# Performance work log

Hardware: AMD Instinct MI355X
Metric: run time of the kernel (lower is better)

Reference implementation:

```python
import jax, jax.numpy as jnp
import numpy as np

VOCAB, D, K = 100000, 300, 5

def setup_inputs() -> dict:
    key = jax.random.key(0)
    ks = jax.random.split(key, 12)
    B, BAG, L = 64, 16, 128
    token_ids = jax.random.randint(ks[0], (B * BAG, L), 0, VOCAB)
    mention_rep = jax.random.normal(ks[1], (B, BAG, D), dtype=jnp.float32)
    s = 0.05
    emb = jax.random.normal(ks[2], (VOCAB, D), dtype=jnp.float32)
    W1 = jax.random.normal(ks[3], (D, D), dtype=jnp.float32) * s
    b1 = jnp.zeros((D,), jnp.float32)
    conv_w = jax.random.normal(ks[4], (D, D, K), dtype=jnp.float32) * s  # [out, in, k]
    conv_b = jnp.zeros((D,), jnp.float32)
    W2 = jax.random.normal(ks[5], (2 * D, D), dtype=jnp.float32) * s
    b2 = jnp.zeros((D,), jnp.float32)
    W3 = jax.random.normal(ks[6], (D, D), dtype=jnp.float32) * s
    b3 = jnp.zeros((D,), jnp.float32)
    return {"token_ids": token_ids, "mention_rep": mention_rep, "emb": emb,
            "W1": W1, "b1": b1, "conv_w": conv_w, "conv_b": conv_b,
            "W2": W2, "b2": b2, "W3": W3, "b3": b3}

def reference(token_ids, mention_rep, emb, W1, b1, conv_w, conv_b, W2, b2, W3, b3):
    # fused gather+pad: [N, L, D]
    x = emb[token_ids]
    # lin1
    x = x @ W1 + b1
    # conv1d over time, VALID, stride 1: NCH layout
    xc = jnp.transpose(x, (0, 2, 1))  # [N, D, L]
    y = jax.lax.conv_general_dilated(xc, conv_w, (1,), 'VALID',
                                     dimension_numbers=('NCH', 'OIH', 'NCH'))
    y = y + conv_b[None, :, None]
    cnn_out = jnp.max(y, axis=-1)  # [N, D]
    m = mention_rep.reshape(mention_rep.shape[0] * mention_rep.shape[1], -1)  # dropout = identity (eval)
    concat = jnp.concatenate([cnn_out, m], axis=-1)
    h = jnp.tanh(concat @ W2 + b2)
    out = h @ W3 + b3  # dropout = identity (eval)
    return out
```

## Files before the change

### kernel.cpp

```cpp
#include <hip/hip_runtime.h>


#define DD   300
#define LL   128
#define TOUT 124
#define CH   16
#define XR   20
#define NSTG 8
#define BLK  320
#define KS     19
#define SLABP  6080
#define ROWP   20
#define WS_G1_OFF  0
#define WS_CV_OFF  194560
#define WS_NEEDED  1167360
#define NPH        114

typedef __attribute__((ext_vector_type(8))) _Float16 f16x8;
typedef __attribute__((ext_vector_type(4))) _Float16 f16x4;
typedef __attribute__((ext_vector_type(4))) float f32x4;
typedef __attribute__((ext_vector_type(16))) float f32x16;
typedef unsigned int   u32;
typedef unsigned short u16;
typedef __attribute__((ext_vector_type(4))) u32 u32x4;

__device__ __forceinline__ float b2f(u16 u) {
    union { float f; u32 i; } x; x.i = ((u32)u) << 16; return x.f;
}
__device__ __forceinline__ u16 f2bu(float f) {
    union { float f; u32 i; } x; x.f = f;
    u32 r = x.i + 0x7FFFu + ((x.i >> 16) & 1u);
    return (u16)(r >> 16);
}
__device__ __forceinline__ float ld(const void* p, size_t idx, int is32) {
    return is32 ? ((const float*)p)[idx] : b2f(((const u16*)p)[idx]);
}
__device__ __forceinline__ int sniff_is32(const void* W1) {
    int cnt = 0;
    const u32* w1raw = (const u32*)W1;
    for (int i = 0; i < 64; ++i) {
        u32 e = (w1raw[i] >> 7) & 0xFFu;
        cnt += (e >= 100u && e <= 126u) ? 1 : 0;
    }
    return (cnt < 32) ? 1 : 0;
}

__device__ __forceinline__ void barrier_lgkm() {
    asm volatile("s_waitcnt lgkmcnt(0)" ::: "memory");
    __builtin_amdgcn_s_barrier();
}

__device__ __forceinline__ void unit_decomp(int u, int& o, int& kq) {
    kq = (u >= 912) ? 3 : (u >= 608) ? 2 : (u >= 304) ? 1 : 0;
    o  = u - 304 * kq;
}
__device__ __forceinline__ void g1_load(const float* W1f, int kk, int o, int kq, float r[4]) {
    const int kbase = kk * 16 + kq * 4;
    #pragma unroll
    for (int j = 0; j < 4; ++j) {
        const int k = kbase + j;
        r[j] = (k < DD && o < DD) ? W1f[(size_t)k * DD + o] : 0.f;
    }
}
__device__ __forceinline__ void g1_write(_Float16* Ws, int o, int kq, const float r[4]) {
    f16x4 v;
    #pragma unroll
    for (int j = 0; j < 4; ++j) v[j] = (_Float16)r[j];
    *(f16x4*)&Ws[o * ROWP + (kq << 2)] = v;
}
__device__ __forceinline__ void cv_load(const float* CWf, int kk, int o, int kq, float r[20]) {
    const int kbase = kk * 16 + kq * 4;
    const bool ok = (o < DD) && (kbase < DD);
    const float4* src = (const float4*)(CWf + (size_t)o * 1500 + kk * 80 + kq * 20);
    #pragma unroll
    for (int i = 0; i < 5; ++i) {
        float4 t = ok ? src[i] : float4{0.f, 0.f, 0.f, 0.f};
        r[4*i] = t.x; r[4*i+1] = t.y; r[4*i+2] = t.z; r[4*i+3] = t.w;
    }
}
__device__ __forceinline__ void cv_write(_Float16* Ws, int o, int kq, const float r[20]) {
    #pragma unroll
    for (int s = 0; s < 5; ++s) {
        f16x4 v;
        #pragma unroll
        for (int j = 0; j < 4; ++j) v[j] = (_Float16)r[j * 5 + s];
        *(f16x4*)&Ws[s * SLABP + o * ROWP + (kq << 2)] = v;
    }
}

__global__ void CNNEncoder_36258113912977_xform(
    const void* W1, const void* conv_w, void* ws)
{
    if (!sniff_is32(W1)) return;
    const int kk = blockIdx.x, part = blockIdx.y, tid = threadIdx.x;

    if (part == 0) {
        const float* W1f = (const float*)W1;
        f16x8* dst = (f16x8*)((char*)ws + WS_G1_OFF) + (size_t)kk * 640;
        for (int g = tid; g < 640; g += 512) {
            const int kc = (g >= 320) ? 1 : 0;
            const int nn = g - kc * 320;
            f16x8 v;
            #pragma unroll
            for (int e = 0; e < 8; ++e) {
                const int k = kk * 16 + kc * 8 + e;
                v[e] = (_Float16)((k < DD && nn < DD) ? W1f[(size_t)k * DD + nn] : 0.f);
            }
            dst[g] = v;
        }
    } else {
        const int s = part - 1;
        const float* CWf = (const float*)conv_w;
        f16x8* dst = (f16x8*)((char*)ws + WS_CV_OFF) + (size_t)kk * 3200 + (size_t)s * 640;
        for (int g = tid; g < 640; g += 512) {
            const int kc = (g >= 320) ? 1 : 0;
            const int nn = g - kc * 320;
            f16x8 v;
            #pragma unroll
            for (int e = 0; e < 8; ++e) {
                const int k = kk * 16 + kc * 8 + e;
                v[e] = (_Float16)((k < DD && nn < DD)
                        ? CWf[(size_t)nn * 1500 + (size_t)k * 5 + s] : 0.f);
            }
            dst[g] = v;
        }
    }
}

#define STAGE_PH(P, Q) do {                                                 \
    if (stager) {                                                           \
        const int wr_ = (P) + 5;                                            \
        if (wr_ < NPH) *(u32x4*)&ring[(wr_ % 6) * 5120 + sg * 8] = Q;       \
        const int lp_ = (P) + 7;                                            \
        if (lp_ < NPH) Q = ((const u32x4*)ws)[(size_t)lp_ * 640 + sg];      \
    }                                                                       \
} while (0)

#define PH_BODY(P, SROW, KKC, Q) do {                                       \
    STAGE_PH((P), Q);                                                       \
    const int c_ = 2 * (KKC) + lh;                                          \
    const int row_ = mrow0 + l31 + (SROW);                                  \
    const f16x8 a_ = *(const f16x8*)&XB[row_ * 320 + ((c_ ^ (row_ & 7)) << 3)]; \
    const _Float16* bp_ = &ring[((P) % 6) * 5120 + lh * 2560];              \
    __builtin_amdgcn_s_setprio(1);                                          \
    { const f16x8 b_ = *(const f16x8*)&bp_[nn0 * 8];                        \
      acc0 = __builtin_amdgcn_mfma_f32_32x32x16_f16(a_, b_, acc0, 0, 0, 0); } \
    { const f16x8 b_ = *(const f16x8*)&bp_[nn1 * 8];                        \
      acc1 = __builtin_amdgcn_mfma_f32_32x32x16_f16(a_, b_, acc1, 0, 0, 0); } \
    if (nt3) { const f16x8 b_ = *(const f16x8*)&bp_[nn2 * 8];               \
      acc2 = __builtin_amdgcn_mfma_f32_32x32x16_f16(a_, b_, acc2, 0, 0, 0); } \
    __builtin_amdgcn_s_setprio(0);                                          \
    barrier_lgkm();                                                         \
} while (0)

#define PH_G1(KK, Q)    PH_BODY((KK), 0, (KK), Q)
#define PH_CV(KK, S, Q) PH_BODY(19 + (KK) * 5 + (S), (S), (KK), Q)

#define EPI_TILE(ACC, TILE) do {                                            \
    const int col_ = (TILE) * 32 + l31;                                     \
    const float bb_ = (col_ < DD) ? b1f[col_] : 0.f;                        \
    const int cc_ = col_ >> 3, c7_ = col_ & 7;                              \
    _Pragma("unroll")                                                       \
    for (int q_ = 0; q_ < 4; ++q_) {                                        \
        _Pragma("unroll")                                                   \
        for (int r_ = 0; r_ < 4; ++r_) {                                    \
            const int row_ = mrow0 + q_ * 8 + 4 * lh + r_;                  \
            XB[row_ * 320 + ((cc_ ^ (row_ & 7)) << 3) + c7_]                \
                = (_Float16)(ACC[4 * q_ + r_] + bb_);                       \
        } }                                                                 \
} while (0)

#define MAX_TILE(ACC, TILE) do {                                            \
    float m_ = -3.0e38f;                                                    \
    _Pragma("unroll")                                                       \
    for (int q_ = 0; q_ < 4; ++q_) {                                        \
        if (!(wm == 3 && q_ == 3)) {                                        \
            _Pragma("unroll")                                               \
            for (int r_ = 0; r_ < 4; ++r_) m_ = fmaxf(m_, ACC[4 * q_ + r_]); \
        } else if (lh == 0) {                                               \
            _Pragma("unroll")                                               \
            for (int r_ = 0; r_ < 4; ++r_) m_ = fmaxf(m_, ACC[12 + r_]);    \
        } }                                                                 \
    m_ = fmaxf(m_, __shfl_xor(m_, 32));                                     \
    if (lh == 0) pmax4[wm][(TILE) * 32 + l31] = m_;                         \
} while (0)

__global__ __launch_bounds__(1024, 4) void CNNEncoder_36258113912977_kernel(
    const int* __restrict__ tok, const void* mention, const void* emb,
    const void* W1, const void* b1, const void* conv_w, const void* conv_b,
    const void* W2, const void* b2, const void* W3, const void* b3,
    void* out, const void* ws)
{
    if (!sniff_is32(W1)) return;

    __shared__ __align__(16) _Float16 XB[132 * 320];
    __shared__ __align__(16) _Float16 ring[6 * 5120];
    __shared__ float pmax4[4][320];
    __shared__ float cbuf[2 * DD];
    __shared__ float hpart[2][DD];
    __shared__ float hbuf[DD];

    const int n = blockIdx.x, tid = threadIdx.x;
    const int w   = tid >> 6;
    const int l   = tid & 63;
    const int l31 = l & 31, lh = l >> 5;
    const int wm  = w >> 2;
    const int wn  = w & 3;
    const int mrow0 = wm * 32;
    const bool nt3 = (wn < 2);
    const int nn0 = wn * 32 + l31;
    const int nn1 = nn0 + 128;
    const int nn2 = nn0 + 256;
    const bool stager = (w < 10);
    const int sg = w * 64 + l;
    const int* trow = tok + (size_t)n * LL;

    u32x4 qE, qO;
    u32x4 pre0, pre1, pre2, pre3, pre4;

    if (stager) {
        const u32x4* wsv = (const u32x4*)ws;
        pre0 = wsv[sg];          pre1 = wsv[640 + sg];
        pre2 = wsv[1280 + sg];   pre3 = wsv[1920 + sg];
        pre4 = wsv[2560 + sg];
        qE   = wsv[3200 + sg];
        qO   = wsv[3840 + sg];
    }

    for (int i = tid; i < 132 * 160; i += 1024) ((u32*)XB)[i] = 0u;
    barrier_lgkm();

    {
        const int r = tid >> 3, q = tid & 7;
        const float* erow = (const float*)emb + (size_t)trow[r] * DD;
        for (int c = q; c < 38; c += 8) {
            f16x8 v;
            if (c < 37) {
                const float4 f0 = *(const float4*)(erow + 8 * c);
                const float4 f1 = *(const float4*)(erow + 8 * c + 4);
                v[0]=(_Float16)f0.x; v[1]=(_Float16)f0.y;
                v[2]=(_Float16)f0.z; v[3]=(_Float16)f0.w;
                v[4]=(_Float16)f1.x; v[5]=(_Float16)f1.y;
                v[6]=(_Float16)f1.z; v[7]=(_Float16)f1.w;
            } else {
                const float4 f0 = *(const float4*)(erow + 296);
                v[0]=(_Float16)f0.x; v[1]=(_Float16)f0.y;
                v[2]=(_Float16)f0.z; v[3]=(_Float16)f0.w;
                v[4]=(_Float16)0.f; v[5]=(_Float16)0.f;
                v[6]=(_Float16)0.f; v[7]=(_Float16)0.f;
            }
            const int p = c ^ (r & 7);
            *(f16x8*)&XB[r * 320 + (p << 3)] = v;
        }
    }

    if (stager) {
        *(u32x4*)&ring[0 * 5120 + sg * 8] = pre0;
        *(u32x4*)&ring[1 * 5120 + sg * 8] = pre1;
        *(u32x4*)&ring[2 * 5120 + sg * 8] = pre2;
        *(u32x4*)&ring[3 * 5120 + sg * 8] = pre3;
        *(u32x4*)&ring[4 * 5120 + sg * 8] = pre4;
    }
    barrier_lgkm();

    f32x16 acc0, acc1, acc2;
    #pragma unroll
    for (int j = 0; j < 16; ++j) { acc0[j] = 0.f; acc1[j] = 0.f; acc2[j] = 0.f; }

    for (int kk = 0; kk < 18; kk += 2) {
        PH_G1(kk,     qE);
        PH_G1(kk + 1, qO);
    }
    PH_G1(18, qE);

    {
        const float* b1f = (const float*)b1;
        EPI_TILE(acc0, wn);
        EPI_TILE(acc1, wn + 4);
        if (nt3) EPI_TILE(acc2, wn + 8);
    }
    barrier_lgkm();

    #pragma unroll
    for (int j = 0; j < 16; ++j) { acc0[j] = 0.f; acc1[j] = 0.f; acc2[j] = 0.f; }

    for (int kk = 0; kk < 18; kk += 2) {
        PH_CV(kk, 0, qO);  PH_CV(kk, 1, qE);
        PH_CV(kk, 2, qO);  PH_CV(kk, 3, qE);
        PH_CV(kk, 4, qO);
        PH_CV(kk + 1, 0, qE);  PH_CV(kk + 1, 1, qO);
        PH_CV(kk + 1, 2, qE);  PH_CV(kk + 1, 3, qO);
        PH_CV(kk + 1, 4, qE);
    }
    PH_CV(18, 0, qO);  PH_CV(18, 1, qE);
    PH_CV(18, 2, qO);  PH_CV(18, 3, qE);
    PH_CV(18, 4, qO);

    MAX_TILE(acc0, wn);
    MAX_TILE(acc1, wn + 4);
    if (nt3) MAX_TILE(acc2, wn + 8);
    __syncthreads();

    if (tid < DD) {
        float m = fmaxf(fmaxf(pmax4[0][tid], pmax4[1][tid]),
                        fmaxf(pmax4[2][tid], pmax4[3][tid]));
        cbuf[tid]      = m + ((const float*)conv_b)[tid];
        cbuf[DD + tid] = ((const float*)mention)[(size_t)n * DD + tid];
    }
    __syncthreads();

    if (tid < 2 * DD) {
        const int part = (tid >= DD) ? 1 : 0;
        const int j = tid - part * DD;
        const float* W2f = (const float*)W2;
        const int c0 = part * DD;
        float a0 = 0.f, a1 = 0.f, a2 = 0.f, a3 = 0.f;
        for (int c = c0; c < c0 + DD; c += 4) {
            a0 += cbuf[c]     * W2f[(size_t)c * DD + j];
            a1 += cbuf[c + 1] * W2f[(size_t)(c + 1) * DD + j];
            a2 += cbuf[c + 2] * W2f[(size_t)(c + 2) * DD + j];
            a3 += cbuf[c + 3] * W2f[(size_t)(c + 3) * DD + j];
        }
        hpart[part][j] = (a0 + a1) + (a2 + a3);
    }
    __syncthreads();
    if (tid < DD)
        hbuf[tid] = tanhf(((const float*)b2)[tid] + hpart[0][tid] + hpart[1][tid]);
    __syncthreads();

    if (tid < 2 * DD) {
        const int part = (tid >= DD) ? 1 : 0;
        const int j = tid - part * DD;
        const float* W3f = (const float*)W3;
        const int c0 = part * 150;
        float a0 = 0.f, a1 = 0.f;
        for (int c = c0; c < c0 + 150; c += 2) {
            a0 += hbuf[c]     * W3f[(size_t)c * DD + j];
            a1 += hbuf[c + 1] * W3f[(size_t)(c + 1) * DD + j];
        }
        hpart[part][j] = a0 + a1;
    }
    __syncthreads();
    if (tid < DD)
        ((float*)out)[(size_t)n * DD + tid]
            = ((const float*)b3)[tid] + hpart[0][tid] + hpart[1][tid];
}

__global__ __launch_bounds__(512, 2) void CNNEncoder_36258113912977_nows(
    const int* __restrict__ tok, const void* mention, const void* emb,
    const void* W1, const void* b1, const void* conv_w, const void* conv_b,
    const void* W2, const void* b2, const void* W3, const void* b3,
    void* out)
{
    if (!sniff_is32(W1)) return;

    __shared__ __align__(16) _Float16 XB[132 * 320];
    __shared__ __align__(16) _Float16 Ws[5 * SLABP];
    __shared__ float pmax2[2][304];
    __shared__ float cbuf[2 * DD];
    __shared__ float hbuf[DD];

    const int n = blockIdx.x, tid = threadIdx.x;
    const int w   = tid >> 6;
    const int l   = tid & 63;
    const int l15 = l & 15, lg = l >> 4;
    const int wm  = w >> 2;
    const int wn  = w & 3;
    const int ntw   = (wn < 3) ? 5 : 4;
    const int nbase = wn * 80;
    const int mrow0 = wm * 64;
    const int* trow = tok + (size_t)n * LL;
    const float* W1f = (const float*)W1;
    const float* CWf = (const float*)conv_w;

    int o0, kq0, o1, kq1, o2, kq2;
    unit_decomp(tid, o0, kq0);
    unit_decomp(512 + tid, o1, kq1);
    const bool act2 = (l < 24);
    unit_decomp(1024 + w * 24 + (l < 24 ? l : 0), o2, kq2);

    for (int i = tid; i < 132 * 160; i += 512) ((u32*)XB)[i] = 0u;
    __syncthreads();

    {
        const int r = tid >> 2, q = tid & 3;
        const float* erow = (const float*)emb + (size_t)trow[r] * DD;
        for (int c = q; c < 38; c += 4) {
            f16x8 v;
            if (c < 37) {
                const float4 f0 = *(const float4*)(erow + 8 * c);
                const float4 f1 = *(const float4*)(erow + 8 * c + 4);
                v[0]=(_Float16)f0.x; v[1]=(_Float16)f0.y;
                v[2]=(_Float16)f0.z; v[3]=(_Float16)f0.w;
                v[4]=(_Float16)f1.x; v[5]=(_Float16)f1.y;
                v[6]=(_Float16)f1.z; v[7]=(_Float16)f1.w;
            } else {
                const float4 f0 = *(const float4*)(erow + 296);
                v[0]=(_Float16)f0.x; v[1]=(_Float16)f0.y;
                v[2]=(_Float16)f0.z; v[3]=(_Float16)f0.w;
                v[4]=(_Float16)0.f; v[5]=(_Float16)0.f;
                v[6]=(_Float16)0.f; v[7]=(_Float16)0.f;
            }
            const int p = c ^ (r & 7);
            *(f16x8*)&XB[r * 320 + (p << 3)] = v;
        }
    }

    f32x4 acc[4][5];
    const f32x4 vzero = {0.f, 0.f, 0.f, 0.f};
    #pragma unroll
    for (int mt = 0; mt < 4; ++mt)
        #pragma unroll
        for (int nt = 0; nt < 5; ++nt) acc[mt][nt] = vzero;

    float g1a[4], g1b[4], g1c[4];
    float cfa[20], cfb[20], cfc[20];

    g1_load(W1f, 0, o0, kq0, g1a);
    g1_load(W1f, 0, o1, kq1, g1b);
    if (act2) g1_load(W1f, 0, o2, kq2, g1c);
    __syncthreads();

    for (int kk = 0; kk < KS; ++kk) {
        g1_write(Ws, o0, kq0, g1a);
        g1_write(Ws, o1, kq1, g1b);
        if (act2) g1_write(Ws, o2, kq2, g1c);
        barrier_lgkm();
        if (kk + 1 < KS) {
            g1_load(W1f, kk + 1, o0, kq0, g1a);
            g1_load(W1f, kk + 1, o1, kq1, g1b);
            if (act2) g1_load(W1f, kk + 1, o2, kq2, g1c);
        } else {
            cv_load(CWf, 0, o0, kq0, cfa);
            cv_load(CWf, 0, o1, kq1, cfb);
            if (act2) cv_load(CWf, 0, o2, kq2, cfc);
        }
        {
            f16x4 af[4];
            #pragma unroll
            for (int mt = 0; mt < 4; ++mt) {
                const int row = mrow0 + mt * 16 + l15;
                const int c = (kk << 1) + (lg >> 1);
                af[mt] = *(const f16x4*)&XB[row * 320 + ((c ^ (row & 7)) << 3) + ((lg & 1) << 2)];
            }
            #pragma unroll
            for (int nt = 0; nt < 5; ++nt) {
                if (nt < ntw) {
                    const int nn = nbase + nt * 16 + l15;
                    const f16x4 b = *(const f16x4*)&Ws[nn * ROWP + (lg << 2)];
                    #pragma unroll
                    for (int mt = 0; mt < 4; ++mt)
                        acc[mt][nt] = __builtin_amdgcn_mfma_f32_16x16x16f16(af[mt], b, acc[mt][nt], 0, 0, 0);
                }
            }
        }
        __builtin_amdgcn_s_barrier();
    }

    {
        const float* b1f = (const float*)b1;
        #pragma unroll
        for (int nt = 0; nt < 5; ++nt) {
            if (nt < ntw) {
                const int col = nbase + nt * 16 + l15;
                const float bb = (col < DD) ? b1f[col] : 0.f;
                #pragma unroll
                for (int mt = 0; mt < 4; ++mt) {
                    #pragma unroll
                    for (int j = 0; j < 4; ++j) {
                        const int row = mrow0 + mt * 16 + (lg << 2) + j;
                        XB[row * 320 + (((col >> 3) ^ (row & 7)) << 3) + (col & 7)]
                            = (_Float16)(acc[mt][nt][j] + bb);
                    }
                }
            }
        }
    }

    #pragma unroll
    for (int mt = 0; mt < 4; ++mt)
        #pragma unroll
        for (int nt = 0; nt < 5; ++nt) acc[mt][nt] = vzero;

    for (int kk = 0; kk < KS; ++kk) {
        cv_write(Ws, o0, kq0, cfa);
        cv_write(Ws, o1, kq1, cfb);
        if (act2) cv_write(Ws, o2, kq2, cfc);
        barrier_lgkm();
        if (kk + 1 < KS) {
            cv_load(CWf, kk + 1, o0, kq0, cfa);
            cv_load(CWf, kk + 1, o1, kq1, cfb);
            if (act2) cv_load(CWf, kk + 1, o2, kq2, cfc);
        }
        #pragma unroll
        for (int s = 0; s < 5; ++s) {
            f16x4 af[4];
            #pragma unroll
            for (int mt = 0; mt < 4; ++mt) {
                const int row = mrow0 + mt * 16 + l15 + s;
                const int c = (kk << 1) + (lg >> 1);
                af[mt] = *(const f16x4*)&XB[row * 320 + ((c ^ (row & 7)) << 3) + ((lg & 1) << 2)];
            }
            #pragma unroll
            for (int nt = 0; nt < 5; ++nt) {
                if (nt < ntw) {
                    const int nn = nbase + nt * 16 + l15;
                    const f16x4 b = *(const f16x4*)&Ws[s * SLABP + nn * ROWP + (lg << 2)];
                    #pragma unroll
                    for (int mt = 0; mt < 4; ++mt)
                        acc[mt][nt] = __builtin_amdgcn_mfma_f32_16x16x16f16(af[mt], b, acc[mt][nt], 0, 0, 0);
                }
            }
        }
        __builtin_amdgcn_s_barrier();
    }

    #pragma unroll
    for (int nt = 0; nt < 5; ++nt) {
        if (nt < ntw) {
            float m = -3.0e38f;
            #pragma unroll
            for (int mt = 0; mt < 4; ++mt) {
                #pragma unroll
                for (int j = 0; j < 4; ++j) {
                    const int t = mrow0 + mt * 16 + (lg << 2) + j;
                    if (t < TOUT) m = fmaxf(m, acc[mt][nt][j]);
                }
            }
            m = fmaxf(m, __shfl_xor(m, 16));
            m = fmaxf(m, __shfl_xor(m, 32));
            if (lg == 0) pmax2[wm][nbase + nt * 16 + l15] = m;
        }
    }
    __syncthreads();

    if (tid < DD) {
        const float m = fmaxf(pmax2[0][tid], pmax2[1][tid]);
        cbuf[tid]      = m + ((const float*)conv_b)[tid];
        cbuf[DD + tid] = ((const float*)mention)[(size_t)n * DD + tid];
    }
    __syncthreads();

    if (tid < DD) {
        const float* W2f = (const float*)W2;
        float a0 = 0.f, a1 = 0.f, a2 = 0.f, a3 = 0.f;
        for (int c = 0; c < 2 * DD; c += 4) {
            a0 += cbuf[c]     * W2f[(size_t)c * DD + tid];
            a1 += cbuf[c + 1] * W2f[(size_t)(c + 1) * DD + tid];
            a2 += cbuf[c + 2] * W2f[(size_t)(c + 2) * DD + tid];
            a3 += cbuf[c + 3] * W2f[(size_t)(c + 3) * DD + tid];
        }
        hbuf[tid] = tanhf(((const float*)b2)[tid] + (a0 + a1) + (a2 + a3));
    }
    __syncthreads();

    if (tid < DD) {
        const float* W3f = (const float*)W3;
        float a0 = 0.f, a1 = 0.f;
        for (int c = 0; c < DD; c += 2) {
            a0 += hbuf[c]     * W3f[(size_t)c * DD + tid];
            a1 += hbuf[c + 1] * W3f[(size_t)(c + 1) * DD + tid];
        }
        ((float*)out)[(size_t)n * DD + tid] = ((const float*)b3)[tid] + a0 + a1;
    }
}

__global__ void CNNEncoder_36258113912977_fallback(
    const int* tok, const void* mention, const void* emb,
    const void* W1, const void* b1, const void* conv_w, const void* conv_b,
    const void* W2, const void* b2, const void* W3, const void* b3,
    void* out)
{
    __shared__ float g[XR * DD];
    __shared__ float xh[XR * DD];
    __shared__ float concat[2 * DD];
    __shared__ float hbuf[DD];

    const int n = blockIdx.x, tid = threadIdx.x;
    const int* trow = tok + (size_t)n * LL;

    if (sniff_is32(W1)) return;
    const int is32 = 0;

    float mmax = -3.0e38f;

    for (int stage = 0; stage < NSTG; ++stage) {
        const int tbase = stage * CH;
        __syncthreads();

        for (int i = tid; i < XR * DD; i += BLK) {
            int r = i / DD, c = i - (i / DD) * DD;
            int gr = tbase + r; if (gr > 127) gr = 127;
            g[i] = ld(emb, (size_t)trow[gr] * DD + c, is32);
        }
        __syncthreads();

        if (tid < DD) {
            float acc[XR];
            #pragma unroll
            for (int r = 0; r < XR; ++r) acc[r] = 0.f;
            for (int k = 0; k < DD; ++k) {
                float wv = ld(W1, (size_t)k * DD + tid, is32);
                #pragma unroll
                for (int r = 0; r < XR; ++r) acc[r] += g[r * DD + k] * wv;
            }
            float bb = ld(b1, tid, is32);
            #pragma unroll
            for (int r = 0; r < XR; ++r) xh[r * DD + tid] = acc[r] + bb;
        }
        __syncthreads();

        if (tid < DD) {
            float y[CH];
            #pragma unroll
            for (int t = 0; t < CH; ++t) y[t] = 0.f;
            const size_t cwoff = (size_t)tid * (DD * 5);
            for (int k = 0; k < DD; ++k) {
                #pragma unroll
                for (int s = 0; s < 5; ++s) {
                    float wv = ld(conv_w, cwoff + k * 5 + s, is32);
                    #pragma unroll
                    for (int t = 0; t < CH; ++t)
                        y[t] += xh[(t + s) * DD + k] * wv;
                }
            }
            #pragma unroll
            for (int t = 0; t < CH; ++t) {
                int tt = tbase + t;
                if (tt < TOUT) mmax = fmaxf(mmax, y[t]);
            }
        }
    }

    __syncthreads();
    if (tid < DD) {
        concat[tid]      = mmax + ld(conv_b, tid, is32);
        concat[DD + tid] = ld(mention, (size_t)n * DD + tid, is32);
    }
    __syncthreads();

    if (tid < DD) {
        float a = ld(b2, tid, is32);
        for (int c = 0; c < 2 * DD; ++c)
            a += concat[c] * ld(W2, (size_t)c * DD + tid, is32);
        hbuf[tid] = tanhf(a);
    }
    __syncthreads();

    if (tid < DD) {
        float a = ld(b3, tid, is32);
        for (int c = 0; c < DD; ++c)
            a += hbuf[c] * ld(W3, (size_t)c * DD + tid, is32);
        ((u16*)out)[(size_t)n * DD + tid] = f2bu(a);
    }
}

extern "C" void kernel_launch(void* const* d_in, const int* in_sizes, int n_in,
                              void* d_out, int out_size, void* d_ws, size_t ws_size,
                              hipStream_t stream)
{
    if (ws_size >= (size_t)WS_NEEDED && d_ws != nullptr) {
        CNNEncoder_36258113912977_xform<<<dim3(19, 6), 512, 0, stream>>>(
            d_in[3], d_in[5], d_ws);
        CNNEncoder_36258113912977_kernel<<<1024, 1024, 0, stream>>>(
            (const int*)d_in[0], d_in[1], d_in[2], d_in[3], d_in[4], d_in[5],
            d_in[6], d_in[7], d_in[8], d_in[9], d_in[10], d_out, d_ws);
    } else {
        CNNEncoder_36258113912977_nows<<<1024, 512, 0, stream>>>(
            (const int*)d_in[0], d_in[1], d_in[2], d_in[3], d_in[4], d_in[5],
            d_in[6], d_in[7], d_in[8], d_in[9], d_in[10], d_out);
    }
    CNNEncoder_36258113912977_fallback<<<1024, BLK, 0, stream>>>(
        (const int*)d_in[0], d_in[1], d_in[2], d_in[3], d_in[4], d_in[5],
        d_in[6], d_in[7], d_in[8], d_in[9], d_in[10], d_out);
}
```

Measured before the change: 520.0 us.

## Split each sequence across two 512-thread blocks with a separate tail kernel

New measurement: 590.0 us. 1.13x slower.

```diff
diff --git a/kernel.cpp b/kernel.cpp
--- a/kernel.cpp
+++ b/kernel.cpp
@@ -4,20 +4,13 @@
 #define DD   300
 #define LL   128
 #define TOUT 124
-#define CH   16
-#define XR   20
-#define NSTG 8
 #define BLK  320
-#define KS     19
-#define SLABP  6080
-#define ROWP   20
-#define WS_G1_OFF  0
-#define WS_CV_OFF  194560
-#define WS_NEEDED  1167360
-#define NPH        114
+#define WS_SMALL    1167360
+#define WS_PMAX_OFF 1167360
+#define WS_BIG      3788800
+#define NPH         114
 
 typedef __attribute__((ext_vector_type(8))) _Float16 f16x8;
-typedef __attribute__((ext_vector_type(4))) _Float16 f16x4;
 typedef __attribute__((ext_vector_type(4))) float f32x4;
 typedef __attribute__((ext_vector_type(16))) float f32x16;
 typedef unsigned int   u32;
@@ -44,48 +37,9 @@
     }
     return (cnt < 32) ? 1 : 0;
 }
-
 __device__ __forceinline__ void barrier_lgkm() {
     asm volatile("s_waitcnt lgkmcnt(0)" ::: "memory");
     __builtin_amdgcn_s_barrier();
-}
-
-__device__ __forceinline__ void unit_decomp(int u, int& o, int& kq) {
-    kq = (u >= 912) ? 3 : (u >= 608) ? 2 : (u >= 304) ? 1 : 0;
-    o  = u - 304 * kq;
-}
-__device__ __forceinline__ void g1_load(const float* W1f, int kk, int o, int kq, float r[4]) {
-    const int kbase = kk * 16 + kq * 4;
-    #pragma unroll
-    for (int j = 0; j < 4; ++j) {
-        const int k = kbase + j;
-        r[j] = (k < DD && o < DD) ? W1f[(size_t)k * DD + o] : 0.f;
-    }
-}
-__device__ __forceinline__ void g1_write(_Float16* Ws, int o, int kq, const float r[4]) {
-    f16x4 v;
-    #pragma unroll
-    for (int j = 0; j < 4; ++j) v[j] = (_Float16)r[j];
-    *(f16x4*)&Ws[o * ROWP + (kq << 2)] = v;
-}
-__device__ __forceinline__ void cv_load(const float* CWf, int kk, int o, int kq, float r[20]) {
-    const int kbase = kk * 16 + kq * 4;
-    const bool ok = (o < DD) && (kbase < DD);
-    const float4* src = (const float4*)(CWf + (size_t)o * 1500 + kk * 80 + kq * 20);
-    #pragma unroll
-    for (int i = 0; i < 5; ++i) {
-        float4 t = ok ? src[i] : float4{0.f, 0.f, 0.f, 0.f};
-        r[4*i] = t.x; r[4*i+1] = t.y; r[4*i+2] = t.z; r[4*i+3] = t.w;
-    }
-}
-__device__ __forceinline__ void cv_write(_Float16* Ws, int o, int kq, const float r[20]) {
-    #pragma unroll
-    for (int s = 0; s < 5; ++s) {
-        f16x4 v;
-        #pragma unroll
-        for (int j = 0; j < 4; ++j) v[j] = (_Float16)r[j * 5 + s];
-        *(f16x4*)&Ws[s * SLABP + o * ROWP + (kq << 2)] = v;
-    }
 }
 
 __global__ void CNNEncoder_36258113912977_xform(
@@ -93,10 +47,9 @@
 {
     if (!sniff_is32(W1)) return;
     const int kk = blockIdx.x, part = blockIdx.y, tid = threadIdx.x;
-
     if (part == 0) {
         const float* W1f = (const float*)W1;
-        f16x8* dst = (f16x8*)((char*)ws + WS_G1_OFF) + (size_t)kk * 640;
+        f16x8* dst = (f16x8*)ws + (size_t)kk * 640;
         for (int g = tid; g < 640; g += 512) {
             const int kc = (g >= 320) ? 1 : 0;
             const int nn = g - kc * 320;
@@ -111,7 +64,7 @@
     } else {
         const int s = part - 1;
         const float* CWf = (const float*)conv_w;
-        f16x8* dst = (f16x8*)((char*)ws + WS_CV_OFF) + (size_t)kk * 3200 + (size_t)s * 640;
+        f16x8* dst = (f16x8*)((char*)ws + 194560) + (size_t)kk * 3200 + (size_t)s * 640;
         for (int g = tid; g < 640; g += 512) {
             const int kc = (g >= 320) ? 1 : 0;
             const int nn = g - kc * 320;
@@ -127,21 +80,54 @@
     }
 }
 
-#define STAGE_PH(P, Q) do {                                                 \
-    if (stager) {                                                           \
-        const int wr_ = (P) + 5;                                            \
-        if (wr_ < NPH) *(u32x4*)&ring[(wr_ % 6) * 5120 + sg * 8] = Q;       \
-        const int lp_ = (P) + 7;                                            \
-        if (lp_ < NPH) Q = ((const u32x4*)ws)[(size_t)lp_ * 640 + sg];      \
+__device__ __forceinline__ float clean_dot(const _Float16* XB, const float* W1f,
+                                           const float* b1f, int idx) {
+    const int rr = (idx >= 900) ? 3 : (idx >= 600) ? 2 : (idx >= 300) ? 1 : 0;
+    const int col = idx - 300 * rr;
+    const int row = 64 + rr;
+    float a = b1f[col];
+    for (int kc = 0; kc < 37; ++kc) {
+        const f16x8 xv = *(const f16x8*)&XB[row * 320 + ((kc ^ (row & 7)) << 3)];
+        #pragma unroll
+        for (int e = 0; e < 8; ++e)
+            a += (float)xv[e] * W1f[(size_t)(8 * kc + e) * DD + col];
+    }
+    {
+        const f16x8 xv = *(const f16x8*)&XB[row * 320 + ((37 ^ (row & 7)) << 3)];
+        #pragma unroll
+        for (int e = 0; e < 4; ++e)
+            a += (float)xv[e] * W1f[(size_t)(296 + e) * DD + col];
+    }
+    return a;
+}
+__device__ __forceinline__ void clean_wr(_Float16* XB, int idx, float v) {
+    const int rr = (idx >= 900) ? 3 : (idx >= 600) ? 2 : (idx >= 300) ? 1 : 0;
+    const int col = idx - 300 * rr;
+    const int row = 64 + rr;
+    XB[row * 320 + (((col >> 3) ^ (row & 7)) << 3) + (col & 7)] = (_Float16)v;
+}
+
+#define STG2(P, Q, QX) do {                                                 \
+    const int wr_ = (P) + 2;                                                \
+    if (wr_ < NPH) {                                                        \
+        _Float16* d_ = &ring[(wr_ % 3) * 5120];                             \
+        *(u32x4*)&d_[tid * 8] = Q;                                          \
+        if (tid < 128) *(u32x4*)&d_[(512 + tid) * 8] = QX;                  \
+    }                                                                       \
+    const int lp_ = (P) + 4;                                                \
+    if (lp_ < NPH) {                                                        \
+        const u32x4* s_ = (const u32x4*)ws + (size_t)lp_ * 640;             \
+        Q = s_[tid];                                                        \
+        if (tid < 128) QX = s_[512 + tid];                                  \
     }                                                                       \
 } while (0)
 
-#define PH_BODY(P, SROW, KKC, Q) do {                                       \
-    STAGE_PH((P), Q);                                                       \
+#define PH2(P, SROW, KKC, Q, QX) do {                                       \
+    STG2((P), Q, QX);                                                       \
     const int c_ = 2 * (KKC) + lh;                                          \
-    const int row_ = mrow0 + l31 + (SROW);                                  \
+    const int row_ = (wm << 5) + l31 + (SROW);                              \
     const f16x8 a_ = *(const f16x8*)&XB[row_ * 320 + ((c_ ^ (row_ & 7)) << 3)]; \
-    const _Float16* bp_ = &ring[((P) % 6) * 5120 + lh * 2560];              \
+    const _Float16* bp_ = &ring[((P) % 3) * 5120 + lh * 2560];              \
     __builtin_amdgcn_s_setprio(1);                                          \
     { const f16x8 b_ = *(const f16x8*)&bp_[nn0 * 8];                        \
       acc0 = __builtin_amdgcn_mfma_f32_32x32x16_f16(a_, b_, acc0, 0, 0, 0); } \
@@ -153,10 +139,10 @@
     barrier_lgkm();                                                         \
 } while (0)
 
-#define PH_G1(KK, Q)    PH_BODY((KK), 0, (KK), Q)
-#define PH_CV(KK, S, Q) PH_BODY(19 + (KK) * 5 + (S), (S), (KK), Q)
-
-#define EPI_TILE(ACC, TILE) do {                                            \
+#define PH2_G1(KK, Q, QX)    PH2((KK), 0, (KK), Q, QX)
+#define PH2_CV(KK, S, Q, QX) PH2(19 + (KK) * 5 + (S), (S), (KK), Q, QX)
+
+#define EPI2(ACC, TILE) do {                                                \
     const int col_ = (TILE) * 32 + l31;                                     \
     const float bb_ = (col_ < DD) ? b1f[col_] : 0.f;                        \
     const int cc_ = col_ >> 3, c7_ = col_ & 7;                              \
@@ -164,17 +150,17 @@
     for (int q_ = 0; q_ < 4; ++q_) {                                        \
         _Pragma("unroll")                                                   \
         for (int r_ = 0; r_ < 4; ++r_) {                                    \
-            const int row_ = mrow0 + q_ * 8 + 4 * lh + r_;                  \
+            const int row_ = (wm << 5) + q_ * 8 + 4 * lh + r_;              \
             XB[row_ * 320 + ((cc_ ^ (row_ & 7)) << 3) + c7_]                \
                 = (_Float16)(ACC[4 * q_ + r_] + bb_);                       \
         } }                                                                 \
 } while (0)
 
-#define MAX_TILE(ACC, TILE) do {                                            \
+#define MAX2(ACC, TILE) do {                                                \
     float m_ = -3.0e38f;                                                    \
     _Pragma("unroll")                                                       \
     for (int q_ = 0; q_ < 4; ++q_) {                                        \
-        if (!(wm == 3 && q_ == 3)) {                                        \
+        if (!(half && wm == 1 && q_ == 3)) {                                \
             _Pragma("unroll")                                               \
             for (int r_ = 0; r_ < 4; ++r_) m_ = fmaxf(m_, ACC[4 * q_ + r_]); \
         } else if (lh == 0) {                                               \
@@ -182,84 +168,89 @@
             for (int r_ = 0; r_ < 4; ++r_) m_ = fmaxf(m_, ACC[12 + r_]);    \
         } }                                                                 \
     m_ = fmaxf(m_, __shfl_xor(m_, 32));                                     \
-    if (lh == 0) pmax4[wm][(TILE) * 32 + l31] = m_;                         \
+    if (lh == 0) pmax2[wm][(TILE) * 32 + l31] = m_;                         \
 } while (0)
 
-__global__ __launch_bounds__(1024, 4) void CNNEncoder_36258113912977_kernel(
+__global__ __launch_bounds__(512, 4) void CNNEncoder_36258113912977_kernel(
     const int* __restrict__ tok, const void* mention, const void* emb,
     const void* W1, const void* b1, const void* conv_w, const void* conv_b,
     const void* W2, const void* b2, const void* W3, const void* b3,
-    void* out, const void* ws)
+    void* out, void* ws)
 {
     if (!sniff_is32(W1)) return;
 
-    __shared__ __align__(16) _Float16 XB[132 * 320];
-    __shared__ __align__(16) _Float16 ring[6 * 5120];
-    __shared__ float pmax4[4][320];
-    __shared__ float cbuf[2 * DD];
-    __shared__ float hpart[2][DD];
-    __shared__ float hbuf[DD];
-
-    const int n = blockIdx.x, tid = threadIdx.x;
+    __shared__ __align__(16) _Float16 XB[72 * 320];
+    __shared__ __align__(16) _Float16 ring[3 * 5120];
+    __shared__ float pmax2[2][320];
+
+    const int bx = blockIdx.x;
+    const int n = bx >> 1, half = bx & 1;
+    const int tid = threadIdx.x;
     const int w   = tid >> 6;
     const int l   = tid & 63;
     const int l31 = l & 31, lh = l >> 5;
     const int wm  = w >> 2;
     const int wn  = w & 3;
-    const int mrow0 = wm * 32;
     const bool nt3 = (wn < 2);
     const int nn0 = wn * 32 + l31;
     const int nn1 = nn0 + 128;
     const int nn2 = nn0 + 256;
-    const bool stager = (w < 10);
-    const int sg = w * 64 + l;
     const int* trow = tok + (size_t)n * LL;
-
-    u32x4 qE, qO;
-    u32x4 pre0, pre1, pre2, pre3, pre4;
-
-    if (stager) {
+    const float* b1f = (const float*)b1;
+    const float* W1f = (const float*)W1;
+
+    u32x4 qE, qEx, qO, qOx;
+    u32x4 p0a, p0b, p1a, p1b;
+
+    {
         const u32x4* wsv = (const u32x4*)ws;
-        pre0 = wsv[sg];          pre1 = wsv[640 + sg];
-        pre2 = wsv[1280 + sg];   pre3 = wsv[1920 + sg];
-        pre4 = wsv[2560 + sg];
-        qE   = wsv[3200 + sg];
-        qO   = wsv[3840 + sg];
-    }
-
-    for (int i = tid; i < 132 * 160; i += 1024) ((u32*)XB)[i] = 0u;
+        p0a = wsv[tid];           p1a = wsv[640 + tid];
+        qE  = wsv[1280 + tid];    qO  = wsv[1920 + tid];
+        if (tid < 128) {
+            p0b = wsv[512 + tid];   p1b = wsv[1152 + tid];
+            qEx = wsv[1792 + tid];  qOx = wsv[2432 + tid];
+        }
+    }
+
+    for (int i = tid; i < 72 * 160; i += 512) ((u32*)XB)[i] = 0u;
     barrier_lgkm();
 
     {
-        const int r = tid >> 3, q = tid & 7;
-        const float* erow = (const float*)emb + (size_t)trow[r] * DD;
-        for (int c = q; c < 38; c += 8) {
-            f16x8 v;
-            if (c < 37) {
-                const float4 f0 = *(const float4*)(erow + 8 * c);
-                const float4 f1 = *(const float4*)(erow + 8 * c + 4);
-                v[0]=(_Float16)f0.x; v[1]=(_Float16)f0.y;
-                v[2]=(_Float16)f0.z; v[3]=(_Float16)f0.w;
-                v[4]=(_Float16)f1.x; v[5]=(_Float16)f1.y;
-                v[6]=(_Float16)f1.z; v[7]=(_Float16)f1.w;
-            } else {
-                const float4 f0 = *(const float4*)(erow + 296);
-                v[0]=(_Float16)f0.x; v[1]=(_Float16)f0.y;
-                v[2]=(_Float16)f0.z; v[3]=(_Float16)f0.w;
-                v[4]=(_Float16)0.f; v[5]=(_Float16)0.f;
-                v[6]=(_Float16)0.f; v[7]=(_Float16)0.f;
-            }
-            const int p = c ^ (r & 7);
-            *(f16x8*)&XB[r * 320 + (p << 3)] = v;
-        }
-    }
-
-    if (stager) {
-        *(u32x4*)&ring[0 * 5120 + sg * 8] = pre0;
-        *(u32x4*)&ring[1 * 5120 + sg * 8] = pre1;
-        *(u32x4*)&ring[2 * 5120 + sg * 8] = pre2;
-        *(u32x4*)&ring[3 * 5120 + sg * 8] = pre3;
-        *(u32x4*)&ring[4 * 5120 + sg * 8] = pre4;
+        const int nrows = half ? 64 : 68;
+        const int r0 = tid >> 3, q0 = tid & 7;
+        #pragma unroll
+        for (int pass = 0; pass < 2; ++pass) {
+            const int r = pass ? (64 + (tid >> 3)) : r0;
+            const int q = pass ? (tid & 7) : q0;
+            if (pass && (tid >= 32 || r >= nrows)) break;
+            const float* erow = (const float*)emb + (size_t)trow[64 * half + r] * DD;
+            for (int c = q; c < 38; c += 8) {
+                f16x8 v;
+                if (c < 37) {
+                    const float4 f0 = *(const float4*)(erow + 8 * c);
+                    const float4 f1 = *(const float4*)(erow + 8 * c + 4);
+                    v[0]=(_Float16)f0.x; v[1]=(_Float16)f0.y;
+                    v[2]=(_Float16)f0.z; v[3]=(_Float16)f0.w;
+                    v[4]=(_Float16)f1.x; v[5]=(_Float16)f1.y;
+                    v[6]=(_Float16)f1.z; v[7]=(_Float16)f1.w;
+                } else {
+                    const float4 f0 = *(const float4*)(erow + 296);
+                    v[0]=(_Float16)f0.x; v[1]=(_Float16)f0.y;
+                    v[2]=(_Float16)f0.z; v[3]=(_Float16)f0.w;
+                    v[4]=(_Float16)0.f; v[5]=(_Float16)0.f;
+                    v[6]=(_Float16)0.f; v[7]=(_Float16)0.f;
+                }
+                const int p = c ^ (r & 7);
+                *(f16x8*)&XB[r * 320 + (p << 3)] = v;
+            }
+        }
+    }
+
+    *(u32x4*)&ring[0 * 5120 + tid * 8] = p0a;
+    *(u32x4*)&ring[1 * 5120 + tid * 8] = p1a;
+    if (tid < 128) {
+        *(u32x4*)&ring[0 * 5120 + (512 + tid) * 8] = p0b;
+        *(u32x4*)&ring[1 * 5120 + (512 + tid) * 8] = p1b;
     }
     barrier_lgkm();
 
@@ -268,16 +259,27 @@
     for (int j = 0; j < 16; ++j) { acc0[j] = 0.f; acc1[j] = 0.f; acc2[j] = 0.f; }
 
     for (int kk = 0; kk < 18; kk += 2) {
-        PH_G1(kk,     qE);
-        PH_G1(kk + 1, qO);
-    }
-    PH_G1(18, qE);
-
-    {
-        const float* b1f = (const float*)b1;
-        EPI_TILE(acc0, wn);
-        EPI_TILE(acc1, wn + 4);
-        if (nt3) EPI_TILE(acc2, wn + 8);
+        PH2_G1(kk,     qE, qEx);
+        PH2_G1(kk + 1, qO, qOx);
+    }
+    PH2_G1(18, qE, qEx);
+
+    EPI2(acc0, wn);
+    EPI2(acc1, wn + 4);
+    if (nt3) EPI2(acc2, wn + 8);
+    __syncthreads();
+
+    if (!half) {
+        const int i0 = tid, i1 = tid + 512, i2 = tid + 1024;
+        float r0 = clean_dot(XB, W1f, b1f, i0);
+        float r1 = clean_dot(XB, W1f, b1f, i1);
+        float r2 = (i2 < 1200) ? clean_dot(XB, W1f, b1f, i2) : 0.f;
+        __syncthreads();
+        clean_wr(XB, i0, r0);
+        clean_wr(XB, i1, r1);
+        if (i2 < 1200) clean_wr(XB, i2, r2);
+    } else {
+        __syncthreads();
     }
     barrier_lgkm();
 
@@ -285,25 +287,43 @@
     for (int j = 0; j < 16; ++j) { acc0[j] = 0.f; acc1[j] = 0.f; acc2[j] = 0.f; }
 
     for (int kk = 0; kk < 18; kk += 2) {
-        PH_CV(kk, 0, qO);  PH_CV(kk, 1, qE);
-        PH_CV(kk, 2, qO);  PH_CV(kk, 3, qE);
-        PH_CV(kk, 4, qO);
-        PH_CV(kk + 1, 0, qE);  PH_CV(kk + 1, 1, qO);
-        PH_CV(kk + 1, 2, qE);  PH_CV(kk + 1, 3, qO);
-        PH_CV(kk + 1, 4, qE);
-    }
-    PH_CV(18, 0, qO);  PH_CV(18, 1, qE);
-    PH_CV(18, 2, qO);  PH_CV(18, 3, qE);
-    PH_CV(18, 4, qO);
-
-    MAX_TILE(acc0, wn);
-    MAX_TILE(acc1, wn + 4);
-    if (nt3) MAX_TILE(acc2, wn + 8);
-    __syncthreads();
+        PH2_CV(kk, 0, qO, qOx);  PH2_CV(kk, 1, qE, qEx);
+        PH2_CV(kk, 2, qO, qOx);  PH2_CV(kk, 3, qE, qEx);
+        PH2_CV(kk, 4, qO, qOx);
+        PH2_CV(kk + 1, 0, qE, qEx);  PH2_CV(kk + 1, 1, qO, qOx);
+        PH2_CV(kk + 1, 2, qE, qEx);  PH2_CV(kk + 1, 3, qO, qOx);
+        PH2_CV(kk + 1, 4, qE, qEx);
+    }
+    PH2_CV(18, 0, qO, qOx);  PH2_CV(18, 1, qE, qEx);
+    PH2_CV(18, 2, qO, qOx);  PH2_CV(18, 3, qE, qEx);
+    PH2_CV(18, 4, qO, qOx);
+
+    MAX2(acc0, wn);
+    MAX2(acc1, wn + 4);
+    if (nt3) MAX2(acc2, wn + 8);
+    __syncthreads();
+
+    if (tid < 320) {
+        const float m = fmaxf(pmax2[0][tid], pmax2[1][tid]);
+        ((float*)((char*)ws + WS_PMAX_OFF))[(size_t)(n * 2 + half) * 320 + tid] = m;
+    }
+}
+
+__global__ void CNNEncoder_36258113912977_tail(
+    const void* mention, const void* conv_b,
+    const void* W2, const void* b2, const void* W3, const void* b3,
+    const void* W1, void* out, const void* ws)
+{
+    if (!sniff_is32(W1)) return;
+    __shared__ float cbuf[2 * DD];
+    __shared__ float hpart[2][DD];
+    __shared__ float hbuf[DD];
+
+    const int n = blockIdx.x, tid = threadIdx.x;
+    const float* pm = (const float*)((const char*)ws + WS_PMAX_OFF) + (size_t)n * 640;
 
     if (tid < DD) {
-        float m = fmaxf(fmaxf(pmax4[0][tid], pmax4[1][tid]),
-                        fmaxf(pmax4[2][tid], pmax4[3][tid]));
+        const float m = fmaxf(pm[tid], pm[320 + tid]);
         cbuf[tid]      = m + ((const float*)conv_b)[tid];
         cbuf[DD + tid] = ((const float*)mention)[(size_t)n * DD + tid];
     }
@@ -346,38 +366,78 @@
             = ((const float*)b3)[tid] + hpart[0][tid] + hpart[1][tid];
 }
 
-__global__ __launch_bounds__(512, 2) void CNNEncoder_36258113912977_nows(
+#define STAGE6(P, Q, QX) do {                                               \
+    const int wr_ = (P) + 5;                                                \
+    if (wr_ < NPH) {                                                        \
+        _Float16* d_ = &ring[(wr_ % 6) * 5120];                             \
+        *(u32x4*)&d_[tid * 8] = Q;                                          \
+        if (tid < 128) *(u32x4*)&d_[(512 + tid) * 8] = QX;                  \
+    }                                                                       \
+    const int lp_ = (P) + 7;                                                \
+    if (lp_ < NPH) {                                                        \
+        const u32x4* s_ = (const u32x4*)ws + (size_t)lp_ * 640;             \
+        Q = s_[tid];                                                        \
+        if (tid < 128) QX = s_[512 + tid];                                  \
+    }                                                                       \
+} while (0)
+
+#define PH6(P, SROW, KKC, Q, QX) do {                                       \
+    STAGE6((P), Q, QX);                                                     \
+    const int phys_ = (P) % 6;                                              \
+    const int c_ = 2 * (KKC) + lh;                                          \
+    const int row_ = mrow0 + l31 + (SROW);                                  \
+    const f16x8 a_ = *(const f16x8*)&XB[row_ * 320 + ((c_ ^ (row_ & 7)) << 3)]; \
+    __builtin_amdgcn_s_setprio(1);                                          \
+    _Pragma("unroll")                                                       \
+    for (int nt_ = 0; nt_ < 5; ++nt_) {                                     \
+        const int nn_ = nbase + nt_ * 32 + l31;                             \
+        const f16x8 b_ = *(const f16x8*)&ring[phys_ * 5120 + lh * 2560 + nn_ * 8]; \
+        acc[nt_] = __builtin_amdgcn_mfma_f32_32x32x16_f16(a_, b_, acc[nt_], 0, 0, 0); \
+    }                                                                       \
+    __builtin_amdgcn_s_setprio(0);                                          \
+    barrier_lgkm();                                                         \
+} while (0)
+
+#define PH6_G1(KK, Q, QX)    PH6((KK), 0, (KK), Q, QX)
+#define PH6_CV(KK, S, Q, QX) PH6(19 + (KK) * 5 + (S), (S), (KK), Q, QX)
+
+__global__ __launch_bounds__(512, 2) void CNNEncoder_36258113912977_mid(
     const int* __restrict__ tok, const void* mention, const void* emb,
     const void* W1, const void* b1, const void* conv_w, const void* conv_b,
     const void* W2, const void* b2, const void* W3, const void* b3,
-    void* out)
+    void* out, const void* ws)
 {
     if (!sniff_is32(W1)) return;
 
     __shared__ __align__(16) _Float16 XB[132 * 320];
-    __shared__ __align__(16) _Float16 Ws[5 * SLABP];
-    __shared__ float pmax2[2][304];
+    __shared__ __align__(16) _Float16 ring[6 * 5120];
+    __shared__ float pmax4[4][320];
     __shared__ float cbuf[2 * DD];
     __shared__ float hbuf[DD];
 
     const int n = blockIdx.x, tid = threadIdx.x;
     const int w   = tid >> 6;
     const int l   = tid & 63;
-    const int l15 = l & 15, lg = l >> 4;
-    const int wm  = w >> 2;
-    const int wn  = w & 3;
-    const int ntw   = (wn < 3) ? 5 : 4;
-    const int nbase = wn * 80;
-    const int mrow0 = wm * 64;
+    const int l31 = l & 31, lh = l >> 5;
+    const int wm  = w >> 1;
+    const int wn  = w & 1;
+    const int nbase = wn * 160;
+    const int mrow0 = wm * 32;
     const int* trow = tok + (size_t)n * LL;
-    const float* W1f = (const float*)W1;
-    const float* CWf = (const float*)conv_w;
-
-    int o0, kq0, o1, kq1, o2, kq2;
-    unit_decomp(tid, o0, kq0);
-    unit_decomp(512 + tid, o1, kq1);
-    const bool act2 = (l < 24);
-    unit_decomp(1024 + w * 24 + (l < 24 ? l : 0), o2, kq2);
+
+    u32x4 qE, qO, qEx, qOx;
+    u32x4 pre[5], prex[5];
+
+    #pragma unroll
+    for (int pl = 0; pl < 5; ++pl) {
+        const u32x4* s_ = (const u32x4*)ws + (size_t)pl * 640;
+        pre[pl] = s_[tid];
+        if (tid < 128) prex[pl] = s_[512 + tid];
+    }
+    { const u32x4* s_ = (const u32x4*)ws + (size_t)5 * 640;
+      qE = s_[tid]; if (tid < 128) qEx = s_[512 + tid]; }
+    { const u32x4* s_ = (const u32x4*)ws + (size_t)6 * 640;
+      qO = s_[tid]; if (tid < 128) qOx = s_[512 + tid]; }
 
     for (int i = tid; i < 132 * 160; i += 512) ((u32*)XB)[i] = 0u;
     __syncthreads();
@@ -406,136 +466,83 @@
         }
     }
 
-    f32x4 acc[4][5];
-    const f32x4 vzero = {0.f, 0.f, 0.f, 0.f};
     #pragma unroll
-    for (int mt = 0; mt < 4; ++mt)
+    for (int pl = 0; pl < 5; ++pl) {
+        *(u32x4*)&ring[pl * 5120 + tid * 8] = pre[pl];
+        if (tid < 128) *(u32x4*)&ring[pl * 5120 + (512 + tid) * 8] = prex[pl];
+    }
+    __syncthreads();
+
+    f32x16 acc[5];
+    #pragma unroll
+    for (int nt = 0; nt < 5; ++nt)
         #pragma unroll
-        for (int nt = 0; nt < 5; ++nt) acc[mt][nt] = vzero;
-
-    float g1a[4], g1b[4], g1c[4];
-    float cfa[20], cfb[20], cfc[20];
-
-    g1_load(W1f, 0, o0, kq0, g1a);
-    g1_load(W1f, 0, o1, kq1, g1b);
-    if (act2) g1_load(W1f, 0, o2, kq2, g1c);
-    __syncthreads();
-
-    for (int kk = 0; kk < KS; ++kk) {
-        g1_write(Ws, o0, kq0, g1a);
-        g1_write(Ws, o1, kq1, g1b);
-        if (act2) g1_write(Ws, o2, kq2, g1c);
-        barrier_lgkm();
-        if (kk + 1 < KS) {
-            g1_load(W1f, kk + 1, o0, kq0, g1a);
-            g1_load(W1f, kk + 1, o1, kq1, g1b);
-            if (act2) g1_load(W1f, kk + 1, o2, kq2, g1c);
-        } else {
-            cv_load(CWf, 0, o0, kq0, cfa);
-            cv_load(CWf, 0, o1, kq1, cfb);
-            if (act2) cv_load(CWf, 0, o2, kq2, cfc);
-        }
-        {
-            f16x4 af[4];
-            #pragma unroll
-            for (int mt = 0; mt < 4; ++mt) {
-                const int row = mrow0 + mt * 16 + l15;
-                const int c = (kk << 1) + (lg >> 1);
-                af[mt] = *(const f16x4*)&XB[row * 320 + ((c ^ (row & 7)) << 3) + ((lg & 1) << 2)];
-            }
-            #pragma unroll
-            for (int nt = 0; nt < 5; ++nt) {
-                if (nt < ntw) {
-                    const int nn = nbase + nt * 16 + l15;
-                    const f16x4 b = *(const f16x4*)&Ws[nn * ROWP + (lg << 2)];
-                    #pragma unroll
-                    for (int mt = 0; mt < 4; ++mt)
-                        acc[mt][nt] = __builtin_amdgcn_mfma_f32_16x16x16f16(af[mt], b, acc[mt][nt], 0, 0, 0);
-                }
-            }
-        }
-        __builtin_amdgcn_s_barrier();
-    }
+        for (int j = 0; j < 16; ++j) acc[nt][j] = 0.f;
+
+    for (int kk = 0; kk < 18; kk += 2) {
+        PH6_G1(kk,     qE, qEx);
+        PH6_G1(kk + 1, qO, qOx);
+    }
+    PH6_G1(18, qE, qEx);
 
     {
         const float* b1f = (const float*)b1;
         #pragma unroll
         for (int nt = 0; nt < 5; ++nt) {
-            if (nt < ntw) {
-                const int col = nbase + nt * 16 + l15;
-                const float bb = (col < DD) ? b1f[col] : 0.f;
+            const int col = nbase + nt * 32 + l31;
+            const float bb = (col < DD) ? b1f[col] : 0.f;
+            const int cc = col >> 3, c7 = col & 7;
+            #pragma unroll
+            for (int q = 0; q < 4; ++q) {
                 #pragma unroll
-                for (int mt = 0; mt < 4; ++mt) {
-                    #pragma unroll
-                    for (int j = 0; j < 4; ++j) {
-                        const int row = mrow0 + mt * 16 + (lg << 2) + j;
-                        XB[row * 320 + (((col >> 3) ^ (row & 7)) << 3) + (col & 7)]
-                            = (_Float16)(acc[mt][nt][j] + bb);
-                    }
+                for (int r = 0; r < 4; ++r) {
+                    const int row = mrow0 + q * 8 + 4 * lh + r;
+                    XB[row * 320 + ((cc ^ (row & 7)) << 3) + c7]
+                        = (_Float16)(acc[nt][4 * q + r] + bb);
                 }
             }
         }
     }
+    __syncthreads();
 
     #pragma unroll
-    for (int mt = 0; mt < 4; ++mt)
+    for (int nt = 0; nt < 5; ++nt)
         #pragma unroll
-        for (int nt = 0; nt < 5; ++nt) acc[mt][nt] = vzero;
-
-    for (int kk = 0; kk < KS; ++kk) {
-        cv_write(Ws, o0, kq0, cfa);
-        cv_write(Ws, o1, kq1, cfb);
-        if (act2) cv_write(Ws, o2, kq2, cfc);
-        barrier_lgkm();
-        if (kk + 1 < KS) {
-            cv_load(CWf, kk + 1, o0, kq0, cfa);
-            cv_load(CWf, kk + 1, o1, kq1, cfb);
-            if (act2) cv_load(CWf, kk + 1, o2, kq2, cfc);
-        }
-        #pragma unroll
-        for (int s = 0; s < 5; ++s) {
-            f16x4 af[4];
-            #pragma unroll
-            for (int mt = 0; mt < 4; ++mt) {
-                const int row = mrow0 + mt * 16 + l15 + s;
-                const int c = (kk << 1) + (lg >> 1);
-                af[mt] = *(const f16x4*)&XB[row * 320 + ((c ^ (row & 7)) << 3) + ((lg & 1) << 2)];
-            }
-            #pragma unroll
-            for (int nt = 0; nt < 5; ++nt) {
-                if (nt < ntw) {
-                    const int nn = nbase + nt * 16 + l15;
-                    const f16x4 b = *(const f16x4*)&Ws[s * SLABP + nn * ROWP + (lg << 2)];
-                    #pragma unroll
-                    for (int mt = 0; mt < 4; ++mt)
-                        acc[mt][nt] = __builtin_amdgcn_mfma_f32_16x16x16f16(af[mt], b, acc[mt][nt], 0, 0, 0);
-                }
-            }
-        }
-        __builtin_amdgcn_s_barrier();
-    }
+        for (int j = 0; j < 16; ++j) acc[nt][j] = 0.f;
+
+    for (int kk = 0; kk < 18; kk += 2) {
+        PH6_CV(kk, 0, qO, qOx);  PH6_CV(kk, 1, qE, qEx);
+        PH6_CV(kk, 2, qO, qOx);  PH6_CV(kk, 3, qE, qEx);
+        PH6_CV(kk, 4, qO, qOx);
+        PH6_CV(kk + 1, 0, qE, qEx);  PH6_CV(kk + 1, 1, qO, qOx);
+        PH6_CV(kk + 1, 2, qE, qEx);  PH6_CV(kk + 1, 3, qO, qOx);
+        PH6_CV(kk + 1, 4, qE, qEx);
+    }
+    PH6_CV(18, 0, qO, qOx);  PH6_CV(18, 1, qE, qEx);
+    PH6_CV(18, 2, qO, qOx);  PH6_CV(18, 3, qE, qEx);
+    PH6_CV(18, 4, qO, qOx);
 
     #pragma unroll
     for (int nt = 0; nt < 5; ++nt) {
-        if (nt < ntw) {
-            float m = -3.0e38f;
-            #pragma unroll
-            for (int mt = 0; mt < 4; ++mt) {
+        float m = -3.0e38f;
+        #pragma unroll
+        for (int q = 0; q < 4; ++q) {
+            if (!(wm == 3 && q == 3)) {
                 #pragma unroll
-                for (int j = 0; j < 4; ++j) {
-                    const int t = mrow0 + mt * 16 + (lg << 2) + j;
-                    if (t < TOUT) m = fmaxf(m, acc[mt][nt][j]);
-                }
-            }
-            m = fmaxf(m, __shfl_xor(m, 16));
-            m = fmaxf(m, __shfl_xor(m, 32));
-            if (lg == 0) pmax2[wm][nbase + nt * 16 + l15] = m;
-        }
+                for (int r = 0; r < 4; ++r) m = fmaxf(m, acc[nt][4 * q + r]);
+            } else if (lh == 0) {
+                #pragma unroll
+                for (int r = 0; r < 4; ++r) m = fmaxf(m, acc[nt][12 + r]);
+            }
+        }
+        m = fmaxf(m, __shfl_xor(m, 32));
+        if (lh == 0) pmax4[wm][nbase + nt * 32 + l31] = m;
     }
     __syncthreads();
 
     if (tid < DD) {
-        const float m = fmaxf(pmax2[0][tid], pmax2[1][tid]);
+        float m = fmaxf(fmaxf(pmax4[0][tid], pmax4[1][tid]),
+                        fmaxf(pmax4[2][tid], pmax4[3][tid]));
         cbuf[tid]      = m + ((const float*)conv_b)[tid];
         cbuf[DD + tid] = ((const float*)mention)[(size_t)n * DD + tid];
     }
@@ -565,11 +572,14 @@
     }
 }
 
+#define CH   16
+#define XR   20
+#define NSTG 8
 __global__ void CNNEncoder_36258113912977_fallback(
     const int* tok, const void* mention, const void* emb,
     const void* W1, const void* b1, const void* conv_w, const void* conv_b,
     const void* W2, const void* b2, const void* W3, const void* b3,
-    void* out)
+    void* out, int force32)
 {
     __shared__ float g[XR * DD];
     __shared__ float xh[XR * DD];
@@ -579,8 +589,8 @@
     const int n = blockIdx.x, tid = threadIdx.x;
     const int* trow = tok + (size_t)n * LL;
 
-    if (sniff_is32(W1)) return;
-    const int is32 = 0;
+    const int is32 = sniff_is32(W1);
+    if (is32 && !force32) return;
 
     float mmax = -3.0e38f;
 
@@ -651,7 +661,9 @@
         float a = ld(b3, tid, is32);
         for (int c = 0; c < DD; ++c)
             a += hbuf[c] * ld(W3, (size_t)c * DD + tid, is32);
-        ((u16*)out)[(size_t)n * DD + tid] = f2bu(a);
+        size_t o = (size_t)n * DD + tid;
+        if (is32) ((float*)out)[o] = a;
+        else      ((u16*)out)[o] = f2bu(a);
     }
 }
 
@@ -659,18 +671,28 @@
                               void* d_out, int out_size, void* d_ws, size_t ws_size,
                               hipStream_t stream)
 {
-    if (ws_size >= (size_t)WS_NEEDED && d_ws != nullptr) {
+    const int small_ok = (d_ws != nullptr) && ws_size >= (size_t)WS_SMALL;
+    const int big_ok   = (d_ws != nullptr) && ws_size >= (size_t)WS_BIG;
+
+    if (small_ok)
         CNNEncoder_36258113912977_xform<<<dim3(19, 6), 512, 0, stream>>>(
             d_in[3], d_in[5], d_ws);
-        CNNEncoder_36258113912977_kernel<<<1024, 1024, 0, stream>>>(
+
+    if (big_ok) {
+        CNNEncoder_36258113912977_kernel<<<2048, 512, 0, stream>>>(
             (const int*)d_in[0], d_in[1], d_in[2], d_in[3], d_in[4], d_in[5],
             d_in[6], d_in[7], d_in[8], d_in[9], d_in[10], d_out, d_ws);
-    } else {
-        CNNEncoder_36258113912977_nows<<<1024, 512, 0, stream>>>(
+        CNNEncoder_36258113912977_tail<<<1024, 640, 0, stream>>>(
+            d_in[1], d_in[6], d_in[7], d_in[8], d_in[9], d_in[10],
+            d_in[3], d_out, d_ws);
+    } else if (small_ok) {
+        CNNEncoder_36258113912977_mid<<<1024, 512, 0, stream>>>(
             (const int*)d_in[0], d_in[1], d_in[2], d_in[3], d_in[4], d_in[5],
-            d_in[6], d_in[7], d_in[8], d_in[9], d_in[10], d_out);
-    }
+            d_in[6], d_in[7], d_in[8], d_in[9], d_in[10], d_out, d_ws);
+    }
+
     CNNEncoder_36258113912977_fallback<<<1024, BLK, 0, stream>>>(
         (const int*)d_in[0], d_in[1], d_in[2], d_in[3], d_in[4], d_in[5],
-        d_in[6], d_in[7], d_in[8], d_in[9], d_in[10], d_out);
-}
+        d_in[6], d_in[7], d_in[8], d_in[9], d_in[10], d_out,
+        small_ok ? 0 : 1);
+}
```
